# Kernel tuning notes

Measured on AMD Instinct MI355X. Metric: run time of the kernel, lower is better.

## Reference

```python
import jax, jax.numpy as jnp
import numpy as np

N = 50000        # nodes
E = 800000       # edges
D_NODE = 128     # input node feature dim
D_HID = 64       # hidden dim
L = 5            # num_layer
G = 128          # number of graphs in batch
BN_EPS = 1e-5


def setup_inputs() -> dict:
    key = jax.random.key(0)
    ks = iter(jax.random.split(key, 64))
    f32 = jnp.float32
    def rn(shape, s=0.05):
        return jax.random.normal(next(ks), shape, dtype=f32) * s
    def rvar(shape):
        return jax.random.uniform(next(ks), shape, dtype=f32) + 0.5
    inp = {}
    inp['x'] = jax.random.normal(next(ks), (N, D_NODE), dtype=f32)
    inp['edge_index'] = jax.random.randint(next(ks), (2, E), 0, N, dtype=jnp.int64)
    inp['batch'] = jnp.sort(jax.random.randint(next(ks), (N,), 0, G, dtype=jnp.int64))
    # layer 0 (conv1): Linear(D_NODE, 2*D_HID) -> BN -> ReLU -> Linear(2*D_HID, D_HID)
    inp['w1_0'] = rn((D_NODE, 2 * D_HID)); inp['b1_0'] = rn((2 * D_HID,))
    inp['ig0'] = rvar((2 * D_HID,)); inp['ib0'] = rn((2 * D_HID,))
    inp['im0'] = rn((2 * D_HID,)); inp['iv0'] = rvar((2 * D_HID,))
    inp['w2_0'] = rn((2 * D_HID, D_HID)); inp['b2_0'] = rn((D_HID,))
    # layers 1..L-1 (stacked): Linear(D_HID, 2*D_HID) -> BN -> ReLU -> Linear(2*D_HID, D_HID)
    M = L - 1
    inp['W1s'] = rn((M, D_HID, 2 * D_HID)); inp['b1s'] = rn((M, 2 * D_HID))
    inp['IG'] = rvar((M, 2 * D_HID)); inp['IB'] = rn((M, 2 * D_HID))
    inp['IM'] = rn((M, 2 * D_HID)); inp['IV'] = rvar((M, 2 * D_HID))
    inp['W2s'] = rn((M, 2 * D_HID, D_HID)); inp['b2s'] = rn((M, D_HID))
    # outer BN per layer (5 layers, all width D_HID)
    inp['OG'] = rvar((L, D_HID)); inp['OB'] = rn((L, D_HID))
    inp['OM'] = rn((L, D_HID)); inp['OV'] = rvar((L, D_HID))
    return inp


def _bn(h, g, b, m, v):
    # eval-mode batch norm with running stats
    return (h - m) * jax.lax.rsqrt(v + BN_EPS) * g + b


def _gin_conv(h, src, dst, W1, b1, ig, ib, im, iv, W2, b2):
    # GINConv, eps=0: MLP(x + sum_{j->i} x_j); scatter-add over edges
    agg = jnp.zeros_like(h).at[dst].add(h[src])  # [N, d]
    z = (h + agg) @ W1 + b1                      # [N, 2*D_HID]
    z = jax.nn.relu(_bn(z, ig, ib, im, iv))
    return z @ W2 + b2                           # [N, D_HID]


def reference(x, edge_index, batch, w1_0, b1_0, ig0, ib0, im0, iv0, w2_0, b2_0,
              W1s, b1s, IG, IB, IM, IV, W2s, b2s, OG, OB, OM, OV):
    src, dst = edge_index[0], edge_index[1]
    # layer 0: conv1 -> BN -> ReLU (dropout = identity in eval)
    h = _gin_conv(x, src, dst, w1_0, b1_0, ig0, ib0, im0, iv0, w2_0, b2_0)
    h = jax.nn.relu(_bn(h, OG[0], OB[0], OM[0], OV[0]))
    # layers 1..L-1 (NB: original relu condition is always true, so relu every layer)
    for i in range(L - 1):
        h = _gin_conv(h, src, dst, W1s[i], b1s[i], IG[i], IB[i], IM[i], IV[i], W2s[i], b2s[i])
        h = jax.nn.relu(_bn(h, OG[i + 1], OB[i + 1], OM[i + 1], OV[i + 1]))
    # readout: global mean pool over graphs
    sums = jax.ops.segment_sum(h, batch, num_segments=G)                      # [G, D_HID]
    cnt = jax.ops.segment_sum(jnp.ones((N,), h.dtype), batch, num_segments=G)  # [G]
    return sums / jnp.maximum(cnt, 1.0)[:, None]
```

## Files before the change

### kernel.cpp

```cpp
#include <hip/hip_runtime.h>
#include <stdint.h>

#define NN 50000
#define NE 800000
#define NG 128
#define BN_EPS 1e-5f

typedef __attribute__((ext_vector_type(8))) __bf16 bf16x8;
typedef __attribute__((ext_vector_type(8))) unsigned short ushort8;
typedef __attribute__((ext_vector_type(4))) float floatx4;

__device__ inline unsigned short f2bf(float f) {
    union { float f; unsigned u; } x; x.f = f;
    unsigned u = x.u;
    return (unsigned short)((u + 0x7fffu + ((u >> 16) & 1u)) >> 16);
}
__device__ inline float bflo(unsigned u) {
    union { unsigned u; float f; } x; x.u = u << 16; return x.f;
}
__device__ inline float bfhi(unsigned u) {
    union { unsigned u; float f; } x; x.u = u & 0xffff0000u; return x.f;
}
__device__ inline unsigned pack_bf2(float a, float b) {
    union { struct { __bf16 x, y; } s; unsigned u; } t;
    t.s.x = (__bf16)a; t.s.y = (__bf16)b; return t.u;
}
__device__ inline bf16x8 as_bf(ushort8 u) {
    union { ushort8 u; bf16x8 b; } x; x.u = u; return x.b;
}


__global__ void hist_kernel(const int* __restrict__ dst, int* __restrict__ deg, int E) {
    int e = blockIdx.x * 256 + threadIdx.x;
    if (e < E) atomicAdd(&deg[dst[e]], 1);
}

__global__ void scan1_kernel(const int* __restrict__ deg, int* __restrict__ row_ptr,
                             int* __restrict__ blocksum, int n) {
    __shared__ int s[256];
    int i = blockIdx.x * 256 + threadIdx.x;
    int v = (i < n) ? deg[i] : 0;
    s[threadIdx.x] = v;
    __syncthreads();
    for (int off = 1; off < 256; off <<= 1) {
        int t = (threadIdx.x >= off) ? s[threadIdx.x - off] : 0;
        __syncthreads();
        s[threadIdx.x] += t;
        __syncthreads();
    }
    if (i < n) row_ptr[i + 1] = s[threadIdx.x];
    if (threadIdx.x == 255) blocksum[blockIdx.x] = s[255];
}

__global__ void scan2_kernel(int* __restrict__ blocksum, int nb) {
    __shared__ int s[256];
    int v = (threadIdx.x < nb) ? blocksum[threadIdx.x] : 0;
    s[threadIdx.x] = v;
    __syncthreads();
    for (int off = 1; off < 256; off <<= 1) {
        int t = (threadIdx.x >= off) ? s[threadIdx.x - off] : 0;
        __syncthreads();
        s[threadIdx.x] += t;
        __syncthreads();
    }
    if (threadIdx.x < nb) blocksum[threadIdx.x] = s[threadIdx.x] - v;
}

__global__ void scan3_kernel(int* __restrict__ row_ptr, const int* __restrict__ blocksum, int n) {
    int i = blockIdx.x * 256 + threadIdx.x;
    if (i < n) row_ptr[i + 1] += blocksum[blockIdx.x];
    if (i == 0) row_ptr[0] = 0;
}

__global__ void fill_kernel(const int* __restrict__ src, const int* __restrict__ dst,
                            const int* __restrict__ row_ptr, int* __restrict__ pos,
                            int* __restrict__ col, int E) {
    int e = blockIdx.x * 256 + threadIdx.x;
    if (e < E) {
        int d = dst[e];
        int p = atomicAdd(&pos[d], 1);
        col[row_ptr[d] + p] = src[e];
    }
}


struct PrepArgs {
    const float* w1[5]; const float* w2[5];
    const float* b1[5]; const float* ig[5]; const float* ib[5];
    const float* im[5]; const float* iv[5]; const float* b2[5];
    const float* og; const float* ob; const float* om; const float* ov;
    unsigned short* w1t[5]; unsigned short* w2t[5];
    float* s1[5]; float* c1[5]; float* s2[5]; float* c2[5];
};

__global__ void prep_kernel(PrepArgs p) {
    int layer = blockIdx.x;
    int K = (layer == 0) ? 128 : 64;
    int kshift = (layer == 0) ? 7 : 6;
    const float* w1 = p.w1[layer];
    unsigned short* w1t = p.w1t[layer];
    for (int idx = threadIdx.x; idx < 128 * K; idx += blockDim.x) {
        int c = idx >> kshift, k = idx & (K - 1);
        w1t[idx] = f2bf(w1[k * 128 + c]);
    }
    const float* w2 = p.w2[layer];
    unsigned short* w2t = p.w2t[layer];
    for (int idx = threadIdx.x; idx < 64 * 128; idx += blockDim.x) {
        int c = idx >> 7, k = idx & 127;
        w2t[idx] = f2bf(w2[k * 64 + c]);
    }
    if (threadIdx.x < 128) {
        int ch = threadIdx.x;
        float s = p.ig[layer][ch] * rsqrtf(p.iv[layer][ch] + BN_EPS);
        p.s1[layer][ch] = s;
        p.c1[layer][ch] = (p.b1[layer][ch] - p.im[layer][ch]) * s + p.ib[layer][ch];
        if (ch < 64) {
            float s2v = p.og[layer * 64 + ch] * rsqrtf(p.ov[layer * 64 + ch] + BN_EPS);
            p.s2[layer][ch] = s2v;
            p.c2[layer][ch] = (p.b2[layer][ch] - p.om[layer * 64 + ch]) * s2v + p.ob[layer * 64 + ch];
        }
    }
}


__global__ void xcvt_kernel(const float* __restrict__ x, unsigned* __restrict__ xb, int npair) {
    int i = blockIdx.x * 256 + threadIdx.x;
    if (i < npair) {
        float2 v = ((const float2*)x)[i];
        xb[i] = pack_bf2(v.x, v.y);
    }
}


__global__ void agg0_kernel(const unsigned* __restrict__ xb, const int* __restrict__ rp,
                            const int* __restrict__ col, unsigned* __restrict__ y, int n) {
    int node = blockIdx.x * 4 + (threadIdx.x >> 6);
    int l = threadIdx.x & 63;
    if (node >= n) return;
    unsigned u = xb[(size_t)node * 64 + l];
    float a0 = bflo(u), a1 = bfhi(u);
    int beg = rp[node], end = rp[node + 1];
    int e = beg;
    for (; e + 2 <= end; e += 2) {
        unsigned v0 = xb[(size_t)col[e] * 64 + l];
        unsigned v1 = xb[(size_t)col[e + 1] * 64 + l];
        a0 += bflo(v0); a1 += bfhi(v0);
        a0 += bflo(v1); a1 += bfhi(v1);
    }
    if (e < end) { unsigned v = xb[(size_t)col[e] * 64 + l]; a0 += bflo(v); a1 += bfhi(v); }
    y[(size_t)node * 64 + l] = pack_bf2(a0, a1);
}

__global__ void agg1_kernel(const unsigned short* __restrict__ h, const int* __restrict__ rp,
                            const int* __restrict__ col, unsigned short* __restrict__ y, int n) {
    int node = blockIdx.x * 8 + (threadIdx.x >> 5);
    int l = threadIdx.x & 31;
    if (node >= n) return;
    const unsigned* hr = (const unsigned*)h;
    unsigned u = hr[(size_t)node * 32 + l];
    float a0 = bflo(u), a1 = bfhi(u);
    int beg = rp[node], end = rp[node + 1];
    int e = beg;
    for (; e + 2 <= end; e += 2) {
        unsigned v0 = hr[(size_t)col[e] * 32 + l];
        unsigned v1 = hr[(size_t)col[e + 1] * 32 + l];
        a0 += bflo(v0); a1 += bfhi(v0);
        a0 += bflo(v1); a1 += bfhi(v1);
    }
    if (e < end) { unsigned v = hr[(size_t)col[e] * 32 + l]; a0 += bflo(v); a1 += bfhi(v); }
    ((unsigned*)y)[(size_t)node * 32 + l] = pack_bf2(a0, a1);
}


template <int K>
__launch_bounds__(256, 3)
__global__ void mlp_mfma(const unsigned short* __restrict__ yb, unsigned short* __restrict__ hb,
                         const unsigned short* __restrict__ w1t,
                         const unsigned short* __restrict__ w2t,
                         const float* __restrict__ s1, const float* __restrict__ c1,
                         const float* __restrict__ s2, const float* __restrict__ c2,
                         int n) {
    __shared__ float zl[64 * 132];
    const int tid = threadIdx.x;
    const int w = tid >> 6;
    const int l = tid & 63;
    const int l15 = l & 15, lg = l >> 4;
    const int node0 = blockIdx.x * 64;

    const int arow = node0 + w * 16 + l15;
    const int arow_c = min(arow, n - 1);
    bf16x8 afr[K / 32];
#pragma unroll
    for (int ks = 0; ks < K / 32; ++ks)
        afr[ks] = as_bf(*(const ushort8*)(yb + (size_t)arow_c * K + ks * 32 + lg * 8));

#pragma unroll
    for (int cc = 0; cc < 8; ++cc) {
        floatx4 acc = {0.f, 0.f, 0.f, 0.f};
#pragma unroll
        for (int ks = 0; ks < K / 32; ++ks) {
            bf16x8 bfr = as_bf(*(const ushort8*)(w1t + (size_t)(cc * 16 + l15) * K + ks * 32 + lg * 8));
            acc = __builtin_amdgcn_mfma_f32_16x16x32_bf16(afr[ks], bfr, acc, 0, 0, 0);
        }
        int ch = cc * 16 + l15;
        float s = s1[ch], c = c1[ch];
#pragma unroll
        for (int r = 0; r < 4; ++r) {
            int row = w * 16 + lg * 4 + r;
            zl[row * 132 + ch] = fmaxf(acc[r] * s + c, 0.f);
        }
    }
    __syncthreads();

    floatx4 acc2[4];
#pragma unroll
    for (int ct = 0; ct < 4; ++ct) acc2[ct] = (floatx4){0.f, 0.f, 0.f, 0.f};

#pragma unroll
    for (int ks = 0; ks < 4; ++ks) {
        const float* zp = &zl[(w * 16 + l15) * 132 + ks * 32 + lg * 8];
        float4 za = *(const float4*)zp;
        float4 zb = *(const float4*)(zp + 4);
        bf16x8 a2;
        a2[0] = (__bf16)za.x; a2[1] = (__bf16)za.y; a2[2] = (__bf16)za.z; a2[3] = (__bf16)za.w;
        a2[4] = (__bf16)zb.x; a2[5] = (__bf16)zb.y; a2[6] = (__bf16)zb.z; a2[7] = (__bf16)zb.w;
#pragma unroll
        for (int ct = 0; ct < 4; ++ct) {
            bf16x8 b2 = as_bf(*(const ushort8*)(w2t + (size_t)(ct * 16 + l15) * 128 + ks * 32 + lg * 8));
            acc2[ct] = __builtin_amdgcn_mfma_f32_16x16x32_bf16(a2, b2, acc2[ct], 0, 0, 0);
        }
    }
    __syncthreads();

    float* Hp = zl + w * 2112;
#pragma unroll
    for (int ct = 0; ct < 4; ++ct) {
        int ch = ct * 16 + l15;
        float s = s2[ch], c = c2[ch];
#pragma unroll
        for (int r = 0; r < 4; ++r)
            Hp[(lg * 4 + r) * 68 + ch] = fmaxf(acc2[ct][r] * s + c, 0.f);
    }
    __syncthreads();

    int nr = l >> 2, ch0 = (l & 3) * 16;
    int node = node0 + w * 16 + nr;
    if (node < n) {
        const float* q = Hp + nr * 68 + ch0;
        ushort8 u0, u1;
#pragma unroll
        for (int j = 0; j < 8; ++j) { union { __bf16 b; unsigned short s; } t; t.b = (__bf16)q[j]; u0[j] = t.s; }
#pragma unroll
        for (int j = 0; j < 8; ++j) { union { __bf16 b; unsigned short s; } t; t.b = (__bf16)q[8 + j]; u1[j] = t.s; }
        *(ushort8*)(hb + (size_t)node * 64 + ch0) = u0;
        *(ushort8*)(hb + (size_t)node * 64 + ch0 + 8) = u1;
    }
}


__global__ void pool_kernel(const unsigned short* __restrict__ h, const int* __restrict__ batch,
                            float* __restrict__ sums, int* __restrict__ cnt, int n) {
    int hw = (blockIdx.x * 256 + threadIdx.x) >> 5;
    int l = threadIdx.x & 31;
    int n0 = hw * 32;
    if (n0 >= n) return;
    int n1 = min(n0 + 32, n);
    const unsigned* hr = (const unsigned*)h;
    float a0 = 0.f, a1 = 0.f; int c = 0;
    int g_cur = batch[n0];
    for (int i = n0; i < n1; ++i) {
        int g = batch[i];
        if (g != g_cur) {
            atomicAdd(&sums[g_cur * 64 + 2 * l], a0);
            atomicAdd(&sums[g_cur * 64 + 2 * l + 1], a1);
            if (l == 0) atomicAdd(&cnt[g_cur], c);
            a0 = a1 = 0.f; c = 0; g_cur = g;
        }
        unsigned u = hr[(size_t)i * 32 + l];
        a0 += bflo(u); a1 += bfhi(u);
        c++;
    }
    atomicAdd(&sums[g_cur * 64 + 2 * l], a0);
    atomicAdd(&sums[g_cur * 64 + 2 * l + 1], a1);
    if (l == 0) atomicAdd(&cnt[g_cur], c);
}

__global__ void finalize_kernel(const float* __restrict__ sums, const int* __restrict__ cnt,
                                float* __restrict__ out) {
    int i = blockIdx.x * 256 + threadIdx.x;
    if (i < NG * 64) {
        float c = (float)cnt[i >> 6];
        out[i] = sums[i] / fmaxf(c, 1.f);
    }
}


extern "C" void kernel_launch(void* const* d_in, const int* in_sizes, int n_in,
                              void* d_out, int out_size, void* d_ws, size_t ws_size,
                              hipStream_t stream) {
    const float* x    = (const float*)d_in[0];
    const int*  ei    = (const int*)d_in[1];
    const int*  batch = (const int*)d_in[2];
    const float* w1_0 = (const float*)d_in[3];
    const float* b1_0 = (const float*)d_in[4];
    const float* ig0  = (const float*)d_in[5];
    const float* ib0  = (const float*)d_in[6];
    const float* im0  = (const float*)d_in[7];
    const float* iv0  = (const float*)d_in[8];
    const float* w2_0 = (const float*)d_in[9];
    const float* b2_0 = (const float*)d_in[10];
    const float* W1s  = (const float*)d_in[11];
    const float* b1s  = (const float*)d_in[12];
    const float* IG   = (const float*)d_in[13];
    const float* IB   = (const float*)d_in[14];
    const float* IM   = (const float*)d_in[15];
    const float* IV   = (const float*)d_in[16];
    const float* W2s  = (const float*)d_in[17];
    const float* b2s  = (const float*)d_in[18];
    const float* OG   = (const float*)d_in[19];
    const float* OB   = (const float*)d_in[20];
    const float* OM   = (const float*)d_in[21];
    const float* OV   = (const float*)d_in[22];
    float* out = (float*)d_out;

    const int N = NN, E = NE;
    const int* src = ei;
    const int* dst = ei + E;

    char* ws = (char*)d_ws;
    size_t off = 0;
    auto alloc = [&](size_t bytes) -> void* {
        void* p = ws + off;
        off += (bytes + 255) & ~(size_t)255;
        return p;
    };
    int*   row_ptr  = (int*)alloc((N + 1) * sizeof(int));
    int*   deg      = (int*)alloc(N * sizeof(int));
    int*   pos      = (int*)alloc(N * sizeof(int));
    int*   blocksum = (int*)alloc(256 * sizeof(int));
    int*   col      = (int*)alloc((size_t)E * sizeof(int));
    unsigned* xb    = (unsigned*)alloc((size_t)N * 64 * 4);
    unsigned short* ybuf = (unsigned short*)alloc((size_t)N * 128 * 2);
    unsigned short* hbuf = (unsigned short*)alloc((size_t)N * 64 * 2);
    unsigned short* w1t  = (unsigned short*)alloc(49152 * 2);
    unsigned short* w2t  = (unsigned short*)alloc(5 * 64 * 128 * 2);
    float* s1 = (float*)alloc(5 * 128 * sizeof(float));
    float* c1 = (float*)alloc(5 * 128 * sizeof(float));
    float* s2 = (float*)alloc(5 * 64 * sizeof(float));
    float* c2 = (float*)alloc(5 * 64 * sizeof(float));
    float* sums = (float*)alloc(NG * 64 * sizeof(float));
    int*   cnt  = (int*)alloc(NG * sizeof(int));

    const int NB = (N + 255) / 256;
    const int EB = (E + 255) / 256;

    hipMemsetAsync(deg, 0, N * sizeof(int), stream);
    hipMemsetAsync(pos, 0, N * sizeof(int), stream);
    hipMemsetAsync(sums, 0, NG * 64 * sizeof(float), stream);
    hipMemsetAsync(cnt, 0, NG * sizeof(int), stream);

    PrepArgs p;
    p.w1[0] = w1_0; p.w2[0] = w2_0; p.b1[0] = b1_0; p.ig[0] = ig0; p.ib[0] = ib0;
    p.im[0] = im0; p.iv[0] = iv0; p.b2[0] = b2_0;
    for (int i = 1; i < 5; ++i) {
        p.w1[i] = W1s + (size_t)(i - 1) * 64 * 128;
        p.w2[i] = W2s + (size_t)(i - 1) * 128 * 64;
        p.b1[i] = b1s + (i - 1) * 128;
        p.ig[i] = IG + (i - 1) * 128; p.ib[i] = IB + (i - 1) * 128;
        p.im[i] = IM + (i - 1) * 128; p.iv[i] = IV + (i - 1) * 128;
        p.b2[i] = b2s + (i - 1) * 64;
    }
    p.og = OG; p.ob = OB; p.om = OM; p.ov = OV;
    p.w1t[0] = w1t;
    for (int i = 1; i < 5; ++i) p.w1t[i] = w1t + 16384 + (size_t)(i - 1) * 8192;
    for (int i = 0; i < 5; ++i) {
        p.w2t[i] = w2t + (size_t)i * 8192;
        p.s1[i] = s1 + i * 128; p.c1[i] = c1 + i * 128;
        p.s2[i] = s2 + i * 64;  p.c2[i] = c2 + i * 64;
    }
    prep_kernel<<<5, 256, 0, stream>>>(p);

    hist_kernel<<<EB, 256, 0, stream>>>(dst, deg, E);
    scan1_kernel<<<NB, 256, 0, stream>>>(deg, row_ptr, blocksum, N);
    scan2_kernel<<<1, 256, 0, stream>>>(blocksum, NB);
    scan3_kernel<<<NB, 256, 0, stream>>>(row_ptr, blocksum, N);
    fill_kernel<<<EB, 256, 0, stream>>>(src, dst, row_ptr, pos, col, E);

    xcvt_kernel<<<(N * 64 + 255) / 256, 256, 0, stream>>>(x, xb, N * 64);

    const int MGB = (N + 63) / 64;

    agg0_kernel<<<(N + 3) / 4, 256, 0, stream>>>(xb, row_ptr, col, (unsigned*)ybuf, N);
    mlp_mfma<128><<<MGB, 256, 0, stream>>>(ybuf, hbuf, p.w1t[0], p.w2t[0],
                                           p.s1[0], p.c1[0], p.s2[0], p.c2[0], N);
    for (int i = 1; i < 5; ++i) {
        agg1_kernel<<<(N + 7) / 8, 256, 0, stream>>>(hbuf, row_ptr, col, ybuf, N);
        mlp_mfma<64><<<MGB, 256, 0, stream>>>(ybuf, hbuf, p.w1t[i], p.w2t[i],
                                              p.s1[i], p.c1[i], p.s2[i], p.c2[i], N);
    }

    pool_kernel<<<NB, 256, 0, stream>>>(hbuf, batch, sums, cnt, N);
    finalize_kernel<<<32, 256, 0, stream>>>(sums, cnt, out);
}
```

Measured before the change: 527.8 us.

## Bucket edges by destination for CSR fill and split aggregation by feature chunks

CSR construction gets a two-pass binning scheme. Edges are first packed into per-256-node buckets, then each bucket is scattered by one block, so the position atomics and column writes land in a small region. Aggregation becomes a single templated kernel that splits the feature dimension into 64-byte column chunks across a second grid dimension, with 4-way unrolled gathers. The aim is to improve cache locality of the gathered rows. The four memsets are merged into one contiguous memset. The 16-bit packing of source indices only works because N is below 65536, and edges are silently dropped if the bucket and overflow capacities are exceeded.

```diff
diff --git a/kernel.cpp b/kernel.cpp
--- a/kernel.cpp
+++ b/kernel.cpp
@@ -5,6 +5,9 @@
 #define NE 800000
 #define NG 128
 #define BN_EPS 1e-5f
+#define NBUCKET 196
+#define BCAP 6144
+#define OCAP 8192
 
 typedef __attribute__((ext_vector_type(8))) __bf16 bf16x8;
 typedef __attribute__((ext_vector_type(8))) unsigned short ushort8;
@@ -72,14 +75,41 @@
     if (i == 0) row_ptr[0] = 0;
 }
 
-__global__ void fill_kernel(const int* __restrict__ src, const int* __restrict__ dst,
+__global__ void binA_kernel(const int* __restrict__ src, const int* __restrict__ dst,
+                            unsigned* __restrict__ bbuf, int* __restrict__ bcnt,
+                            unsigned* __restrict__ obuf, int* __restrict__ ocnt, int E) {
+    int e = blockIdx.x * 256 + threadIdx.x;
+    if (e >= E) return;
+    int d = dst[e], s = src[e];
+    int b = d >> 8;
+    unsigned pk = ((unsigned)d << 16) | (unsigned)s;
+    int p = atomicAdd(&bcnt[b], 1);
+    if (p < BCAP) bbuf[(size_t)b * BCAP + p] = pk;
+    else { int o = atomicAdd(ocnt, 1); if (o < OCAP) obuf[o] = pk; }
+}
+
+__global__ void binB_kernel(const unsigned* __restrict__ bbuf, const int* __restrict__ bcnt,
                             const int* __restrict__ row_ptr, int* __restrict__ pos,
-                            int* __restrict__ col, int E) {
-    int e = blockIdx.x * 256 + threadIdx.x;
-    if (e < E) {
-        int d = dst[e];
-        int p = atomicAdd(&pos[d], 1);
-        col[row_ptr[d] + p] = src[e];
+                            int* __restrict__ col,
+                            const unsigned* __restrict__ obuf, const int* __restrict__ ocnt) {
+    int b = blockIdx.x;
+    if (b < NBUCKET) {
+        int cnt = min(bcnt[b], BCAP);
+        const unsigned* p = bbuf + (size_t)b * BCAP;
+        for (int i = threadIdx.x; i < cnt; i += 256) {
+            unsigned e = p[i];
+            int d = e >> 16, s = e & 0xffff;
+            int q = atomicAdd(&pos[d], 1);
+            col[row_ptr[d] + q] = s;
+        }
+    } else {
+        int cnt = min(*ocnt, OCAP);
+        for (int i = threadIdx.x; i < cnt; i += 256) {
+            unsigned e = obuf[i];
+            int d = e >> 16, s = e & 0xffff;
+            int q = atomicAdd(&pos[d], 1);
+            col[row_ptr[d] + q] = s;
+        }
     }
 }
 
@@ -132,43 +162,32 @@
 }
 
 
-__global__ void agg0_kernel(const unsigned* __restrict__ xb, const int* __restrict__ rp,
-                            const int* __restrict__ col, unsigned* __restrict__ y, int n) {
-    int node = blockIdx.x * 4 + (threadIdx.x >> 6);
-    int l = threadIdx.x & 63;
+template <int DW>
+__global__ void agg_split(const unsigned* __restrict__ hr, const int* __restrict__ rp,
+                          const int* __restrict__ col, unsigned* __restrict__ y, int n) {
+    int node = blockIdx.x * 16 + (threadIdx.x >> 4);
+    int l = threadIdx.x & 15;
     if (node >= n) return;
-    unsigned u = xb[(size_t)node * 64 + l];
+    const unsigned* base = hr + blockIdx.y * 16 + l;
+    unsigned u = base[(size_t)node * DW];
     float a0 = bflo(u), a1 = bfhi(u);
     int beg = rp[node], end = rp[node + 1];
     int e = beg;
-    for (; e + 2 <= end; e += 2) {
-        unsigned v0 = xb[(size_t)col[e] * 64 + l];
-        unsigned v1 = xb[(size_t)col[e + 1] * 64 + l];
+    for (; e + 4 <= end; e += 4) {
+        unsigned v0 = base[(size_t)col[e]     * DW];
+        unsigned v1 = base[(size_t)col[e + 1] * DW];
+        unsigned v2 = base[(size_t)col[e + 2] * DW];
+        unsigned v3 = base[(size_t)col[e + 3] * DW];
         a0 += bflo(v0); a1 += bfhi(v0);
         a0 += bflo(v1); a1 += bfhi(v1);
-    }
-    if (e < end) { unsigned v = xb[(size_t)col[e] * 64 + l]; a0 += bflo(v); a1 += bfhi(v); }
-    y[(size_t)node * 64 + l] = pack_bf2(a0, a1);
-}
-
-__global__ void agg1_kernel(const unsigned short* __restrict__ h, const int* __restrict__ rp,
-                            const int* __restrict__ col, unsigned short* __restrict__ y, int n) {
-    int node = blockIdx.x * 8 + (threadIdx.x >> 5);
-    int l = threadIdx.x & 31;
-    if (node >= n) return;
-    const unsigned* hr = (const unsigned*)h;
-    unsigned u = hr[(size_t)node * 32 + l];
-    float a0 = bflo(u), a1 = bfhi(u);
-    int beg = rp[node], end = rp[node + 1];
-    int e = beg;
-    for (; e + 2 <= end; e += 2) {
-        unsigned v0 = hr[(size_t)col[e] * 32 + l];
-        unsigned v1 = hr[(size_t)col[e + 1] * 32 + l];
-        a0 += bflo(v0); a1 += bfhi(v0);
-        a0 += bflo(v1); a1 += bfhi(v1);
-    }
-    if (e < end) { unsigned v = hr[(size_t)col[e] * 32 + l]; a0 += bflo(v); a1 += bfhi(v); }
-    ((unsigned*)y)[(size_t)node * 32 + l] = pack_bf2(a0, a1);
+        a0 += bflo(v2); a1 += bfhi(v2);
+        a0 += bflo(v3); a1 += bfhi(v3);
+    }
+    for (; e < end; ++e) {
+        unsigned v = base[(size_t)col[e] * DW];
+        a0 += bflo(v); a1 += bfhi(v);
+    }
+    y[(size_t)node * DW + blockIdx.y * 16 + l] = pack_bf2(a0, a1);
 }
 
 
@@ -335,10 +354,18 @@
         return p;
     };
     int*   row_ptr  = (int*)alloc((N + 1) * sizeof(int));
+    int*   blocksum = (int*)alloc(256 * sizeof(int));
+    char*  zbase    = ws + off;
     int*   deg      = (int*)alloc(N * sizeof(int));
     int*   pos      = (int*)alloc(N * sizeof(int));
-    int*   blocksum = (int*)alloc(256 * sizeof(int));
+    int*   bcnt     = (int*)alloc(NBUCKET * sizeof(int));
+    int*   ocnt     = (int*)alloc(sizeof(int));
+    float* sums     = (float*)alloc(NG * 64 * sizeof(float));
+    int*   cnt      = (int*)alloc(NG * sizeof(int));
+    size_t zlen     = (ws + off) - zbase;
     int*   col      = (int*)alloc((size_t)E * sizeof(int));
+    unsigned* bbuf  = (unsigned*)alloc((size_t)NBUCKET * BCAP * 4);
+    unsigned* obuf  = (unsigned*)alloc(OCAP * 4);
     unsigned* xb    = (unsigned*)alloc((size_t)N * 64 * 4);
     unsigned short* ybuf = (unsigned short*)alloc((size_t)N * 128 * 2);
     unsigned short* hbuf = (unsigned short*)alloc((size_t)N * 64 * 2);
@@ -348,16 +375,11 @@
     float* c1 = (float*)alloc(5 * 128 * sizeof(float));
     float* s2 = (float*)alloc(5 * 64 * sizeof(float));
     float* c2 = (float*)alloc(5 * 64 * sizeof(float));
-    float* sums = (float*)alloc(NG * 64 * sizeof(float));
-    int*   cnt  = (int*)alloc(NG * sizeof(int));
 
     const int NB = (N + 255) / 256;
     const int EB = (E + 255) / 256;
 
-    hipMemsetAsync(deg, 0, N * sizeof(int), stream);
-    hipMemsetAsync(pos, 0, N * sizeof(int), stream);
-    hipMemsetAsync(sums, 0, NG * 64 * sizeof(float), stream);
-    hipMemsetAsync(cnt, 0, NG * sizeof(int), stream);
+    hipMemsetAsync(zbase, 0, zlen, stream);
 
     PrepArgs p;
     p.w1[0] = w1_0; p.w2[0] = w2_0; p.b1[0] = b1_0; p.ig[0] = ig0; p.ib[0] = ib0;
@@ -384,17 +406,20 @@
     scan1_kernel<<<NB, 256, 0, stream>>>(deg, row_ptr, blocksum, N);
     scan2_kernel<<<1, 256, 0, stream>>>(blocksum, NB);
     scan3_kernel<<<NB, 256, 0, stream>>>(row_ptr, blocksum, N);
-    fill_kernel<<<EB, 256, 0, stream>>>(src, dst, row_ptr, pos, col, E);
+    binA_kernel<<<EB, 256, 0, stream>>>(src, dst, bbuf, bcnt, obuf, ocnt, E);
+    binB_kernel<<<NBUCKET + 1, 256, 0, stream>>>(bbuf, bcnt, row_ptr, pos, col, obuf, ocnt);
 
     xcvt_kernel<<<(N * 64 + 255) / 256, 256, 0, stream>>>(x, xb, N * 64);
 
     const int MGB = (N + 63) / 64;
-
-    agg0_kernel<<<(N + 3) / 4, 256, 0, stream>>>(xb, row_ptr, col, (unsigned*)ybuf, N);
+    const int ANB = (N + 15) / 16;
+
+    agg_split<64><<<dim3(ANB, 4), 256, 0, stream>>>(xb, row_ptr, col, (unsigned*)ybuf, N);
     mlp_mfma<128><<<MGB, 256, 0, stream>>>(ybuf, hbuf, p.w1t[0], p.w2t[0],
                                            p.s1[0], p.c1[0], p.s2[0], p.c2[0], N);
     for (int i = 1; i < 5; ++i) {
-        agg1_kernel<<<(N + 7) / 8, 256, 0, stream>>>(hbuf, row_ptr, col, ybuf, N);
+        agg_split<32><<<dim3(ANB, 2), 256, 0, stream>>>((const unsigned*)hbuf, row_ptr, col,
+                                                        (unsigned*)ybuf, N);
         mlp_mfma<64><<<MGB, 256, 0, stream>>>(ybuf, hbuf, p.w1t[i], p.w2t[i],
                                               p.s1[i], p.c1[i], p.s2[i], p.c2[i], N);
     }
```

Result: slower. 932.1 us (+76.6%).
